# Optimization experiments

Measured on AMD Instinct MI355X. Metric: run time of the kernel, lower is better.

The kernel has to match this reference:

```python
import jax, jax.numpy as jnp
import numpy as np
from jax import lax

EPS = 1e-5
KH, KW, PAD, DIL = 3, 3, 1, 1


def _bilinear_gather(x, py, px):
    """x: [B,C,H,W]; py/px: [B,K,H,W] float sample coords. Returns [B,C,K,H,W].
    Zero-padding semantics (torchvision deform_conv2d): corners outside the image contribute 0."""
    B, C, H, W = x.shape
    K = py.shape[1]
    y0 = jnp.floor(py)
    x0 = jnp.floor(px)
    wy1 = py - y0
    wy0 = 1.0 - wy1
    wx1 = px - x0
    wx0 = 1.0 - wx1
    xf = x.reshape(B, C, H * W)

    def corner(yc, xc, w):
        valid = (yc >= 0) & (yc <= H - 1) & (xc >= 0) & (xc <= W - 1)
        yi = jnp.clip(yc, 0, H - 1).astype(jnp.int32)
        xi = jnp.clip(xc, 0, W - 1).astype(jnp.int32)
        lin = (yi * W + xi).reshape(B, -1)  # [B, K*H*W]
        v = jax.vmap(lambda xb, lb: xb[:, lb])(xf, lin)  # [B, C, K*H*W]
        return v * (w * valid.astype(x.dtype)).reshape(B, 1, -1)

    out = (corner(y0, x0, wy0 * wx0)
           + corner(y0, x0 + 1.0, wy0 * wx1)
           + corner(y0 + 1.0, x0, wy1 * wx0)
           + corner(y0 + 1.0, x0 + 1.0, wy1 * wx1))
    return out.reshape(B, C, K, H, W)


def _deform_conv(x, offset, w):
    B, C, H, W = x.shape
    K = KH * KW
    off = offset.reshape(B, K, 2, H, W)  # (dy, dx) per kernel tap
    ki = (jnp.arange(K) // KW - PAD).astype(x.dtype)  # kernel row offset (dil=1)
    kj = (jnp.arange(K) % KW - PAD).astype(x.dtype)
    hh = jnp.arange(H).astype(x.dtype)
    ww = jnp.arange(W).astype(x.dtype)
    py = hh[None, None, :, None] + ki[None, :, None, None] + off[:, :, 0]
    px = ww[None, None, None, :] + kj[None, :, None, None] + off[:, :, 1]
    val = _bilinear_gather(x, py, px)  # [B,C,K,H,W]
    return jnp.einsum('bckhw,ock->bohw', val, w.reshape(w.shape[0], C, K))


def _bn(x, gamma, beta, mean, var):
    inv = gamma * lax.rsqrt(var + EPS)
    return x * inv[None, :, None, None] + (beta - mean * inv)[None, :, None, None]


def setup_inputs() -> dict:
    key = jax.random.key(0)
    ks = jax.random.split(key, 12)
    B, C, H, W = 4, 128, 128, 128
    return {
        'x': jax.random.normal(ks[0], (B, C, H, W), jnp.float32),
        'offset': jax.random.normal(ks[1], (B, 2 * KH * KW, H, W), jnp.float32),
        'w1': jax.random.normal(ks[2], (C, C, KH, KW), jnp.float32) * 0.05,
        'bn1_gamma': jax.random.uniform(ks[3], (C,), jnp.float32, 0.5, 1.5),
        'bn1_beta': jax.random.normal(ks[4], (C,), jnp.float32) * 0.1,
        'bn1_mean': jax.random.normal(ks[5], (C,), jnp.float32) * 0.1,
        'bn1_var': jax.random.uniform(ks[6], (C,), jnp.float32, 0.5, 1.5),
        'w2': jax.random.normal(ks[7], (C, C, KH, KW), jnp.float32) * 0.05,
        'bn2_gamma': jax.random.uniform(ks[8], (C,), jnp.float32, 0.5, 1.5),
        'bn2_beta': jax.random.normal(ks[9], (C,), jnp.float32) * 0.1,
        'bn2_mean': jax.random.normal(ks[10], (C,), jnp.float32) * 0.1,
        'bn2_var': jax.random.uniform(ks[11], (C,), jnp.float32, 0.5, 1.5),
    }


def reference(x, offset, w1, bn1_gamma, bn1_beta, bn1_mean, bn1_var,
              w2, bn2_gamma, bn2_beta, bn2_mean, bn2_var):
    identity = x
    out = _deform_conv(x, offset, w1)
    out = jax.nn.relu(_bn(out, bn1_gamma, bn1_beta, bn1_mean, bn1_var))
    out = lax.conv_general_dilated(out, w2, window_strides=(1, 1),
                                   padding=((PAD, PAD), (PAD, PAD)),
                                   dimension_numbers=('NCHW', 'OIHW', 'NCHW'))
    out = _bn(out, bn2_gamma, bn2_beta, bn2_mean, bn2_var)
    out = jax.nn.relu(out + identity)
    return out
```

## Files before the change

kernel.cpp:

```cpp
#include <hip/hip_runtime.h>
#include <hip/hip_fp16.h>
#include <stdint.h>

#define B_ 4
#define C_ 128
#define H_ 128
#define W_ 128
#define HW 16384

typedef _Float16 h8 __attribute__((ext_vector_type(8)));
typedef float f32x16 __attribute__((ext_vector_type(16)));

__device__ __forceinline__ unsigned cvtpk_f16(float lo, float hi) {
    auto r = __builtin_amdgcn_cvt_pkrtz(lo, hi);
    return *(unsigned*)&r;
}

__device__ __forceinline__ unsigned blend_h2(unsigned c0, unsigned c1, unsigned c2, unsigned c3,
                                             __half2 G0, __half2 G1, __half2 G2, __half2 G3) {
    __half2 s = __hmul2(G0, *(__half2*)&c0);
    s = __hfma2(G1, *(__half2*)&c1, s);
    s = __hfma2(G2, *(__half2*)&c2, s);
    s = __hfma2(G3, *(__half2*)&c3, s);
    return *(unsigned*)&s;
}

__device__ __forceinline__ void gll16(const void* g, void* l) {
    __builtin_amdgcn_global_load_lds((const unsigned int*)g, (unsigned int*)l, 16, 0, 0);
}

__global__ __launch_bounds__(256) void prep_all(const float* __restrict__ x,
                                                unsigned short* __restrict__ xh,
                                                const float* __restrict__ w1,
                                                const float* __restrict__ w2,
                                                unsigned short* __restrict__ w1f,
                                                unsigned short* __restrict__ w2f,
                                                unsigned short* __restrict__ o1p,
                                                const float* g1, const float* b1, const float* m1, const float* v1,
                                                const float* g2, const float* b2, const float* m2, const float* v2,
                                                float* inv1, float* sh1, float* inv2, float* sh2) {
    __shared__ unsigned short tile[32][36];
    int blk = blockIdx.x;
    int tid = threadIdx.x;
    if (blk >= 1282) {
        int nb = blk - 1282;
        int wt = nb & 3, ct = (nb >> 2) & 3, h = (nb >> 4) & 127, b = nb >> 11;
        int c = tid >> 3, seg = tid & 7;
        const float* srcp = x + ((size_t)((b * 128 + ct * 32 + c) * 128 + h) * 128) + wt * 32 + seg * 4;
        float4 v = *(const float4*)srcp;
        uint2 pk;
        pk.x = cvtpk_f16(v.x, v.y);
        pk.y = cvtpk_f16(v.z, v.w);
        *(uint2*)&tile[c][seg * 4] = pk;
        __syncthreads();
        int w = tid >> 3, s2 = tid & 7;
        unsigned a0 = tile[s2 * 4 + 0][w];
        unsigned a1 = tile[s2 * 4 + 1][w];
        unsigned a2 = tile[s2 * 4 + 2][w];
        unsigned a3 = tile[s2 * 4 + 3][w];
        uint2 o;
        o.x = (a1 << 16) | a0;
        o.y = (a3 << 16) | a2;
        *(uint2*)(xh + ((size_t)((b * 128 + h) * 128 + wt * 32 + w) * 128) + ct * 32 + s2 * 4) = o;
        return;
    }
    if (blk < 1152) {
        int i = blk * 256 + tid;
        const float* src = w1;
        unsigned short* dst = w1f;
        int j = i;
        if (i >= 147456) { j = i - 147456; src = w2; dst = w2f; }
        int o = j / 1152, rem = j % 1152;
        int c = rem / 9, tap = rem % 9;
        _Float16 hv = (_Float16)src[j];
        int s = o >> 5;
        int ks = c >> 4;
        int l = (o & 31) | (((c >> 3) & 1) << 5);
        int jj = c & 7;
        dst[(((tap * 4 + s) * 8 + ks) * 64 + l) * 8 + jj] = *(unsigned short*)&hv;
    } else if (blk < 1281) {
        int i = (blk - 1152) * 256 + tid;
        if (i < 33024) {
            int chunk = i & 15;
            int pos = i >> 4;
            int b = pos / 516;
            int r = pos % 516;
            int row, col;
            if (r < 130)      { row = 0;   col = r; }
            else if (r < 260) { row = 129; col = r - 130; }
            else { int j = r - 260; row = 1 + (j >> 1); col = (j & 1) * 129; }
            uint4 z = {0u, 0u, 0u, 0u};
            *(uint4*)((char*)o1p + (size_t)((b * 130 + row) * 130 + col) * 256 + chunk * 16) = z;
        }
    } else {
        if (tid < 128) {
            float iv = g1[tid] * rsqrtf(v1[tid] + 1e-5f);
            inv1[tid] = iv; sh1[tid] = b1[tid] - m1[tid] * iv;
        } else {
            int u = tid - 128;
            float iv = g2[u] * rsqrtf(v2[u] + 1e-5f);
            inv2[u] = iv; sh2[u] = b2[u] - m2[u] * iv;
        }
    }
}

__global__ __launch_bounds__(512, 4) void gemm1_k(
    const unsigned short* __restrict__ xh,
    const float* __restrict__ off,
    const unsigned short* __restrict__ w1f,
    const float* __restrict__ inv1,
    const float* __restrict__ sh1,
    unsigned short* __restrict__ out1p) {
    __shared__ __align__(16) char ldsv[2][16384];

    int bid = blockIdx.x;
    int swz = ((bid & 7) << 7) | (bid >> 3);
    int half = swz & 1, h = (swz >> 1) & 127, b = swz >> 8;
    int w0 = half * 64;
    int tid = threadIdx.x;
    int bH = b * H_;
    const char* xb8 = (const char*)xh;

    if (tid < 256) {
        int prow = tid >> 4;
        int seg = tid & 15;
        int sb = seg * 16;

        float dy[4], dx[4];
        unsigned PX[4][4];
        float g[4][4];
        uint4 buf[2][4];

#define OFFLOAD(TT) do { \
    int dyB_ = ((b * 18 + 2 * (TT)) * H_ + h) * W_ + w0; \
    _Pragma("unroll") \
    for (int c_ = 0; c_ < 4; ++c_) { \
        int p_ = prow + c_ * 16; \
        dy[c_] = off[dyB_ + p_]; \
        dx[c_] = off[dyB_ + HW + p_]; \
    } \
} while (0)

#define COORD(TT) do { \
    int kh_ = (TT) / 3 - 1, kw_ = (TT) % 3 - 1; \
    _Pragma("unroll") \
    for (int c_ = 0; c_ < 4; ++c_) { \
        int p_ = prow + c_ * 16; \
        float py_ = (float)(h + kh_) + dy[c_]; \
        float px_ = (float)(w0 + p_ + kw_) + dx[c_]; \
        float y0f_ = floorf(py_), x0f_ = floorf(px_); \
        int y0_ = (int)y0f_, x0_ = (int)x0f_; \
        float wy1_ = py_ - y0f_, wx1_ = px_ - x0f_; \
        float wy0_ = 1.f - wy1_, wx0_ = 1.f - wx1_; \
        int y1_ = y0_ + 1, x1_ = x0_ + 1; \
        g[c_][0] = ((unsigned)y0_ < 128u && (unsigned)x0_ < 128u) ? wy0_ * wx0_ : 0.f; \
        g[c_][1] = ((unsigned)y0_ < 128u && (unsigned)x1_ < 128u) ? wy0_ * wx1_ : 0.f; \
        g[c_][2] = ((unsigned)y1_ < 128u && (unsigned)x0_ < 128u) ? wy1_ * wx0_ : 0.f; \
        g[c_][3] = ((unsigned)y1_ < 128u && (unsigned)x1_ < 128u) ? wy1_ * wx1_ : 0.f; \
        int y0c_ = min(max(y0_, 0), 127), y1c_ = min(max(y1_, 0), 127); \
        int x0c_ = min(max(x0_, 0), 127), x1c_ = min(max(x1_, 0), 127); \
        int r0_ = (bH + y0c_) * W_, r1_ = (bH + y1c_) * W_; \
        PX[c_][0] = (unsigned)((r0_ + x0c_) * 256) + sb; \
        PX[c_][1] = (unsigned)((r0_ + x1c_) * 256) + sb; \
        PX[c_][2] = (unsigned)((r1_ + x0c_) * 256) + sb; \
        PX[c_][3] = (unsigned)((r1_ + x1c_) * 256) + sb; \
    } \
} while (0)

#define ISSUE2(cA, cB) do { \
    _Pragma("unroll") \
    for (int k_ = 0; k_ < 4; ++k_) buf[0][k_] = *(const uint4*)(xb8 + PX[cA][k_]); \
    _Pragma("unroll") \
    for (int k_ = 0; k_ < 4; ++k_) buf[1][k_] = *(const uint4*)(xb8 + PX[cB][k_]); \
} while (0)

#define BLEND1(VP, CC, BI) do { \
    __half2 G0_ = __float2half2_rn(g[CC][0]); \
    __half2 G1_ = __float2half2_rn(g[CC][1]); \
    __half2 G2_ = __float2half2_rn(g[CC][2]); \
    __half2 G3_ = __float2half2_rn(g[CC][3]); \
    uint4 st_; \
    st_.x = blend_h2(buf[BI][0].x, buf[BI][1].x, buf[BI][2].x, buf[BI][3].x, G0_, G1_, G2_, G3_); \
    st_.y = blend_h2(buf[BI][0].y, buf[BI][1].y, buf[BI][2].y, buf[BI][3].y, G0_, G1_, G2_, G3_); \
    st_.z = blend_h2(buf[BI][0].z, buf[BI][1].z, buf[BI][2].z, buf[BI][3].z, G0_, G1_, G2_, G3_); \
    st_.w = blend_h2(buf[BI][0].w, buf[BI][1].w, buf[BI][2].w, buf[BI][3].w, G0_, G1_, G2_, G3_); \
    int row_ = prow + (CC) * 16; \
    *(uint4*)(&ldsv[VP][0] + row_ * 256 + ((seg ^ (row_ & 15)) << 4)) = st_; \
} while (0)

#define GATHER(VP) do { \
    ISSUE2(0, 1); \
    BLEND1(VP, 0, 0); BLEND1(VP, 1, 1); \
    ISSUE2(2, 3); \
    BLEND1(VP, 2, 0); BLEND1(VP, 3, 1); \
} while (0)

        OFFLOAD(0);
        COORD(0);
        GATHER(0);
        OFFLOAD(1);
        __syncthreads();
        for (int t = 0; t < 9; ++t) {
            if (t < 8) {
                COORD(t + 1);
                GATHER((t + 1) & 1);
                if (t < 7) OFFLOAD(t + 2);
            }
            __syncthreads();
        }
#undef OFFLOAD
#undef COORD
#undef ISSUE2
#undef BLEND1
#undef GATHER
    } else {
        int ctid = tid - 256;
        int lane = ctid & 63, wq = ctid >> 6;
        int lp = lane & 31, hi = lane >> 5;
        int lsw = lp & 15;
        int bRow0 = lp * 256;
        int bRow1 = (32 + lp) * 256;

        f32x16 acc0 = {};
        f32x16 acc1 = {};
        h8 wreg[2][8];

        {
            const unsigned short* wb = w1f + wq * 4096 + lane * 8;
            #pragma unroll
            for (int ks = 0; ks < 8; ++ks) wreg[0][ks] = *(const h8*)(wb + ks * 512);
        }
        __syncthreads();
        #pragma unroll
        for (int t = 0; t < 9; ++t) {
            if (t < 8) {
                const unsigned short* wb = w1f + ((t + 1) * 4 + wq) * 4096 + lane * 8;
                #pragma unroll
                for (int ks = 0; ks < 8; ++ks) wreg[(t + 1) & 1][ks] = *(const h8*)(wb + ks * 512);
            }
            const char* vcur = &ldsv[t & 1][0];
            #pragma unroll
            for (int ks = 0; ks < 8; ++ks) {
                int q0 = 2 * ks + hi;
                int sl = (q0 ^ lsw) << 4;
                h8 b0 = *(const h8*)(vcur + bRow0 + sl);
                h8 b1 = *(const h8*)(vcur + bRow1 + sl);
                h8 a = wreg[t & 1][ks];
                acc0 = __builtin_amdgcn_mfma_f32_32x32x16_f16(a, b0, acc0, 0, 0, 0);
                acc1 = __builtin_amdgcn_mfma_f32_32x32x16_f16(a, b1, acc1, 0, 0, 0);
            }
            __syncthreads();
        }

        #pragma unroll
        for (int j = 0; j < 2; ++j) {
            int p = w0 + j * 32 + lp;
            size_t rowbase = (size_t)((b * 130 + h + 1) * 130 + 1 + p) * 128;
            #pragma unroll
            for (int k = 0; k < 4; ++k) {
                int o0 = wq * 32 + k * 8 + hi * 4;
                float4 iv = *(const float4*)(inv1 + o0);
                float4 sv = *(const float4*)(sh1 + o0);
                float e0, e1, e2, e3;
                if (j == 0) {
                    e0 = acc0[4 * k + 0]; e1 = acc0[4 * k + 1];
                    e2 = acc0[4 * k + 2]; e3 = acc0[4 * k + 3];
                } else {
                    e0 = acc1[4 * k + 0]; e1 = acc1[4 * k + 1];
                    e2 = acc1[4 * k + 2]; e3 = acc1[4 * k + 3];
                }
                float v0 = fmaxf(fmaf(e0, iv.x, sv.x), 0.f);
                float v1 = fmaxf(fmaf(e1, iv.y, sv.y), 0.f);
                float v2 = fmaxf(fmaf(e2, iv.z, sv.z), 0.f);
                float v3 = fmaxf(fmaf(e3, iv.w, sv.w), 0.f);
                uint2 pk2;
                pk2.x = cvtpk_f16(v0, v1);
                pk2.y = cvtpk_f16(v2, v3);
                *(uint2*)(out1p + rowbase + o0) = pk2;
            }
        }
    }
}

__global__ __launch_bounds__(512, 4) void gemm2_k(
    const unsigned short* __restrict__ out1p,
    const unsigned short* __restrict__ w2f,
    const unsigned short* __restrict__ xh,
    const float* __restrict__ inv2,
    const float* __restrict__ sh2,
    float* __restrict__ outp) {
    __shared__ __align__(16) char ldsS[33280];

    int bid = blockIdx.x;
    int swz = ((bid & 7) << 6) | (bid >> 3);
    int h = swz & 127, b = swz >> 7;
    int tid = threadIdx.x, lane = tid & 63, wv = tid >> 6;
    int wq = wv >> 1, wp = wv & 1;
    int lp = lane & 31, hi = lane >> 5;
    int lsw = lp & 15;

    f32x16 acc0 = {};
    f32x16 acc1 = {};
    h8 wreg[2][8];

    {
        const unsigned short* wb = w2f + wq * 4096 + lane * 8;
        #pragma unroll
        for (int ks = 0; ks < 8; ++ks) wreg[0][ks] = *(const h8*)(wb + ks * 512);
    }

    #pragma unroll
    for (int t = 0; t < 9; ++t) {
        int kh = t / 3, kw = t % 3;
        if (kw == 0) {
            __syncthreads();
            const char* srow = (const char*)out1p + (size_t)((b * 130 + h + kh) * 130) * 256;
            #pragma unroll
            for (int it = 0; it < 5; ++it) {
                int ci = it * 512 + tid;
                if (ci < 2080) {
                    int r = ci >> 4, q = ci & 15;
                    gll16(srow + r * 256 + ((q ^ (r & 15)) << 4), ldsS + ci * 16);
                }
            }
            __syncthreads();
        }
        if (t < 8) {
            const unsigned short* wb = w2f + ((t + 1) * 4 + wq) * 4096 + lane * 8;
            #pragma unroll
            for (int ks = 0; ks < 8; ++ks) wreg[(t + 1) & 1][ks] = *(const h8*)(wb + ks * 512);
        }
        #pragma unroll
        for (int ks = 0; ks < 8; ++ks) {
            int q0 = 2 * ks + hi;
            int pr0 = wp * 64 + lp + kw;
            int pr1 = pr0 + 32;
            h8 b0 = *(const h8*)(ldsS + pr0 * 256 + ((q0 ^ (pr0 & 15)) << 4));
            h8 b1 = *(const h8*)(ldsS + pr1 * 256 + ((q0 ^ (pr1 & 15)) << 4));
            h8 a = wreg[t & 1][ks];
            acc0 = __builtin_amdgcn_mfma_f32_32x32x16_f16(a, b0, acc0, 0, 0, 0);
            acc1 = __builtin_amdgcn_mfma_f32_32x32x16_f16(a, b1, acc1, 0, 0, 0);
        }
    }

    #pragma unroll
    for (int j = 0; j < 2; ++j) {
        int p = wp * 64 + j * 32 + lp;
        const unsigned short* xrow = xh + (size_t)((b * 128 + h) * 128 + p) * 128;
        #pragma unroll
        for (int k = 0; k < 4; ++k) {
            int o0 = wq * 32 + k * 8 + hi * 4;
            uint2 rx = *(const uint2*)(xrow + o0);
            __half2 hx0 = *(__half2*)&rx.x;
            __half2 hx1 = *(__half2*)&rx.y;
            float x0 = __low2float(hx0), x1 = __high2float(hx0);
            float x2 = __low2float(hx1), x3 = __high2float(hx1);
            float e0, e1, e2, e3;
            if (j == 0) {
                e0 = acc0[4 * k + 0]; e1 = acc0[4 * k + 1];
                e2 = acc0[4 * k + 2]; e3 = acc0[4 * k + 3];
            } else {
                e0 = acc1[4 * k + 0]; e1 = acc1[4 * k + 1];
                e2 = acc1[4 * k + 2]; e3 = acc1[4 * k + 3];
            }
            size_t idx = ((size_t)(b * C_ + o0) * H_ + h) * W_ + p;
            outp[idx]            = fmaxf(fmaf(e0, inv2[o0 + 0], sh2[o0 + 0]) + x0, 0.f);
            outp[idx + HW]       = fmaxf(fmaf(e1, inv2[o0 + 1], sh2[o0 + 1]) + x1, 0.f);
            outp[idx + 2 * HW]   = fmaxf(fmaf(e2, inv2[o0 + 2], sh2[o0 + 2]) + x2, 0.f);
            outp[idx + 3 * HW]   = fmaxf(fmaf(e3, inv2[o0 + 3], sh2[o0 + 3]) + x3, 0.f);
        }
    }
}

extern "C" void kernel_launch(void* const* d_in, const int* in_sizes, int n_in,
                              void* d_out, int out_size, void* d_ws, size_t ws_size,
                              hipStream_t stream) {
    const float* x   = (const float*)d_in[0];
    const float* off = (const float*)d_in[1];
    const float* w1  = (const float*)d_in[2];
    const float* g1  = (const float*)d_in[3];
    const float* b1  = (const float*)d_in[4];
    const float* m1  = (const float*)d_in[5];
    const float* v1  = (const float*)d_in[6];
    const float* w2  = (const float*)d_in[7];
    const float* g2  = (const float*)d_in[8];
    const float* b2  = (const float*)d_in[9];
    const float* m2  = (const float*)d_in[10];
    const float* v2  = (const float*)d_in[11];
    float* outp = (float*)d_out;

    char* ws = (char*)d_ws;
    unsigned short* w1f = (unsigned short*)(ws);
    unsigned short* w2f = (unsigned short*)(ws + 294912);
    float* inv1 = (float*)(ws + 589824);
    float* sh1  = (float*)(ws + 590336);
    float* inv2 = (float*)(ws + 590848);
    float* sh2  = (float*)(ws + 591360);
    unsigned short* xh  = (unsigned short*)(ws + 591872);
    unsigned short* o1p = (unsigned short*)(ws + 17369088);

    prep_all<<<9474, 256, 0, stream>>>(x, xh, w1, w2, w1f, w2f, o1p,
                                       g1, b1, m1, v1, g2, b2, m2, v2,
                                       inv1, sh1, inv2, sh2);
    gemm1_k<<<1024, 512, 0, stream>>>(xh, off, w1f, inv1, sh1, o1p);
    gemm2_k<<<512, 512, 0, stream>>>(o1p, w2f, xh, inv2, sh2, outp);
}
```

Measured before the change: 86.67 us.

## Software-pipeline deformable gather across taps and replace syncthreads with raw barriers

The producer warps now issue all 16 corner loads for the next tap before the barrier and blend them after it. Offsets and bilinear weights are double-buffered and offsets are prefetched two taps ahead, so global gather latency overlaps the MFMA consumer's work on the previous tap. __syncthreads is replaced by explicit s_barrier macros: the producer waits only on LDS/scalar counters (lgkmcnt), so gather loads still in flight across the barrier are not forced to drain. This raises register pressure (four uint4 buffers per corner set, doubled weight arrays) and depends on the hand-built barriers keeping LDS ordering correct.

```diff
diff --git a/kernel.cpp b/kernel.cpp
--- a/kernel.cpp
+++ b/kernel.cpp
@@ -28,6 +28,17 @@
 __device__ __forceinline__ void gll16(const void* g, void* l) {
     __builtin_amdgcn_global_load_lds((const unsigned int*)g, (unsigned int*)l, 16, 0, 0);
 }
+
+#define PBAR() do { \
+    asm volatile("s_waitcnt lgkmcnt(0)" ::: "memory"); \
+    __builtin_amdgcn_s_barrier(); \
+    asm volatile("" ::: "memory"); \
+} while (0)
+#define CBAR() do { \
+    asm volatile("" ::: "memory"); \
+    __builtin_amdgcn_s_barrier(); \
+    asm volatile("" ::: "memory"); \
+} while (0)
 
 __global__ __launch_bounds__(256) void prep_all(const float* __restrict__ x,
                                                 unsigned short* __restrict__ xh,
@@ -126,18 +137,18 @@
         int seg = tid & 15;
         int sb = seg * 16;
 
-        float dy[4], dx[4];
+        float dy[2][4], dx[2][4];
+        float g[2][4][4];
         unsigned PX[4][4];
-        float g[4][4];
-        uint4 buf[2][4];
+        uint4 buf[4][4];
 
 #define OFFLOAD(TT) do { \
     int dyB_ = ((b * 18 + 2 * (TT)) * H_ + h) * W_ + w0; \
     _Pragma("unroll") \
     for (int c_ = 0; c_ < 4; ++c_) { \
         int p_ = prow + c_ * 16; \
-        dy[c_] = off[dyB_ + p_]; \
-        dx[c_] = off[dyB_ + HW + p_]; \
+        dy[(TT) & 1][c_] = off[dyB_ + p_]; \
+        dx[(TT) & 1][c_] = off[dyB_ + HW + p_]; \
     } \
 } while (0)
 
@@ -146,17 +157,17 @@
     _Pragma("unroll") \
     for (int c_ = 0; c_ < 4; ++c_) { \
         int p_ = prow + c_ * 16; \
-        float py_ = (float)(h + kh_) + dy[c_]; \
-        float px_ = (float)(w0 + p_ + kw_) + dx[c_]; \
+        float py_ = (float)(h + kh_) + dy[(TT) & 1][c_]; \
+        float px_ = (float)(w0 + p_ + kw_) + dx[(TT) & 1][c_]; \
         float y0f_ = floorf(py_), x0f_ = floorf(px_); \
         int y0_ = (int)y0f_, x0_ = (int)x0f_; \
         float wy1_ = py_ - y0f_, wx1_ = px_ - x0f_; \
         float wy0_ = 1.f - wy1_, wx0_ = 1.f - wx1_; \
         int y1_ = y0_ + 1, x1_ = x0_ + 1; \
-        g[c_][0] = ((unsigned)y0_ < 128u && (unsigned)x0_ < 128u) ? wy0_ * wx0_ : 0.f; \
-        g[c_][1] = ((unsigned)y0_ < 128u && (unsigned)x1_ < 128u) ? wy0_ * wx1_ : 0.f; \
-        g[c_][2] = ((unsigned)y1_ < 128u && (unsigned)x0_ < 128u) ? wy1_ * wx0_ : 0.f; \
-        g[c_][3] = ((unsigned)y1_ < 128u && (unsigned)x1_ < 128u) ? wy1_ * wx1_ : 0.f; \
+        g[(TT) & 1][c_][0] = ((unsigned)y0_ < 128u && (unsigned)x0_ < 128u) ? wy0_ * wx0_ : 0.f; \
+        g[(TT) & 1][c_][1] = ((unsigned)y0_ < 128u && (unsigned)x1_ < 128u) ? wy0_ * wx1_ : 0.f; \
+        g[(TT) & 1][c_][2] = ((unsigned)y1_ < 128u && (unsigned)x0_ < 128u) ? wy1_ * wx0_ : 0.f; \
+        g[(TT) & 1][c_][3] = ((unsigned)y1_ < 128u && (unsigned)x1_ < 128u) ? wy1_ * wx1_ : 0.f; \
         int y0c_ = min(max(y0_, 0), 127), y1c_ = min(max(y1_, 0), 127); \
         int x0c_ = min(max(x0_, 0), 127), x1c_ = min(max(x1_, 0), 127); \
         int r0_ = (bH + y0c_) * W_, r1_ = (bH + y1c_) * W_; \
@@ -167,52 +178,52 @@
     } \
 } while (0)
 
-#define ISSUE2(cA, cB) do { \
+#define ISSUE_ALL() do { \
     _Pragma("unroll") \
-    for (int k_ = 0; k_ < 4; ++k_) buf[0][k_] = *(const uint4*)(xb8 + PX[cA][k_]); \
+    for (int c_ = 0; c_ < 4; ++c_) \
+        _Pragma("unroll") \
+        for (int k_ = 0; k_ < 4; ++k_) buf[c_][k_] = *(const uint4*)(xb8 + PX[c_][k_]); \
+} while (0)
+
+#define BLEND_ALL(TT) do { \
+    char* vdst_ = &ldsv[(TT) & 1][0]; \
     _Pragma("unroll") \
-    for (int k_ = 0; k_ < 4; ++k_) buf[1][k_] = *(const uint4*)(xb8 + PX[cB][k_]); \
-} while (0)
-
-#define BLEND1(VP, CC, BI) do { \
-    __half2 G0_ = __float2half2_rn(g[CC][0]); \
-    __half2 G1_ = __float2half2_rn(g[CC][1]); \
-    __half2 G2_ = __float2half2_rn(g[CC][2]); \
-    __half2 G3_ = __float2half2_rn(g[CC][3]); \
-    uint4 st_; \
-    st_.x = blend_h2(buf[BI][0].x, buf[BI][1].x, buf[BI][2].x, buf[BI][3].x, G0_, G1_, G2_, G3_); \
-    st_.y = blend_h2(buf[BI][0].y, buf[BI][1].y, buf[BI][2].y, buf[BI][3].y, G0_, G1_, G2_, G3_); \
-    st_.z = blend_h2(buf[BI][0].z, buf[BI][1].z, buf[BI][2].z, buf[BI][3].z, G0_, G1_, G2_, G3_); \
-    st_.w = blend_h2(buf[BI][0].w, buf[BI][1].w, buf[BI][2].w, buf[BI][3].w, G0_, G1_, G2_, G3_); \
-    int row_ = prow + (CC) * 16; \
-    *(uint4*)(&ldsv[VP][0] + row_ * 256 + ((seg ^ (row_ & 15)) << 4)) = st_; \
-} while (0)
-
-#define GATHER(VP) do { \
-    ISSUE2(0, 1); \
-    BLEND1(VP, 0, 0); BLEND1(VP, 1, 1); \
-    ISSUE2(2, 3); \
-    BLEND1(VP, 2, 0); BLEND1(VP, 3, 1); \
+    for (int c_ = 0; c_ < 4; ++c_) { \
+        __half2 G0_ = __float2half2_rn(g[(TT) & 1][c_][0]); \
+        __half2 G1_ = __float2half2_rn(g[(TT) & 1][c_][1]); \
+        __half2 G2_ = __float2half2_rn(g[(TT) & 1][c_][2]); \
+        __half2 G3_ = __float2half2_rn(g[(TT) & 1][c_][3]); \
+        uint4 st_; \
+        st_.x = blend_h2(buf[c_][0].x, buf[c_][1].x, buf[c_][2].x, buf[c_][3].x, G0_, G1_, G2_, G3_); \
+        st_.y = blend_h2(buf[c_][0].y, buf[c_][1].y, buf[c_][2].y, buf[c_][3].y, G0_, G1_, G2_, G3_); \
+        st_.z = blend_h2(buf[c_][0].z, buf[c_][1].z, buf[c_][2].z, buf[c_][3].z, G0_, G1_, G2_, G3_); \
+        st_.w = blend_h2(buf[c_][0].w, buf[c_][1].w, buf[c_][2].w, buf[c_][3].w, G0_, G1_, G2_, G3_); \
+        int row_ = prow + c_ * 16; \
+        *(uint4*)(vdst_ + row_ * 256 + ((seg ^ (row_ & 15)) << 4)) = st_; \
+    } \
 } while (0)
 
         OFFLOAD(0);
         COORD(0);
-        GATHER(0);
+        ISSUE_ALL();
         OFFLOAD(1);
-        __syncthreads();
+        BLEND_ALL(0);
+        COORD(1);
+        ISSUE_ALL();
+        OFFLOAD(2);
+        PBAR();
+
+        #pragma unroll
         for (int t = 0; t < 9; ++t) {
-            if (t < 8) {
-                COORD(t + 1);
-                GATHER((t + 1) & 1);
-                if (t < 7) OFFLOAD(t + 2);
-            }
-            __syncthreads();
+            if (t < 8) BLEND_ALL(t + 1);
+            if (t < 7) { COORD(t + 2); ISSUE_ALL(); }
+            if (t + 3 <= 8) OFFLOAD(t + 3);
+            PBAR();
         }
 #undef OFFLOAD
 #undef COORD
-#undef ISSUE2
-#undef BLEND1
-#undef GATHER
+#undef ISSUE_ALL
+#undef BLEND_ALL
     } else {
         int ctid = tid - 256;
         int lane = ctid & 63, wq = ctid >> 6;
@@ -230,7 +241,7 @@
             #pragma unroll
             for (int ks = 0; ks < 8; ++ks) wreg[0][ks] = *(const h8*)(wb + ks * 512);
         }
-        __syncthreads();
+        CBAR();
         #pragma unroll
         for (int t = 0; t < 9; ++t) {
             if (t < 8) {
@@ -249,7 +260,7 @@
                 acc0 = __builtin_amdgcn_mfma_f32_32x32x16_f16(a, b0, acc0, 0, 0, 0);
                 acc1 = __builtin_amdgcn_mfma_f32_32x32x16_f16(a, b1, acc1, 0, 0, 0);
             }
-            __syncthreads();
+            CBAR();
         }
 
         #pragma unroll
```

Result: faster. 84.18 us (-2.9%).
